# Performance work log

Hardware: AMD Instinct MI355X
Metric: run time of the kernel (lower is better)

## Reference

```python
import jax, jax.numpy as jnp
import numpy as np

N, F_IN, H, OUT, L = 100000, 32, 128, 200, 4
E = 1600000
EPS = 1e-5


def setup_inputs() -> dict:
    key = jax.random.key(0)
    ks = jax.random.split(key, 16)
    glorot = lambda k, shape: jax.random.uniform(k, shape, jnp.float32, -1.0, 1.0) * jnp.sqrt(6.0 / (shape[0] + shape[1]))
    return {
        'x': jax.random.normal(ks[0], (N, F_IN), jnp.float32),
        'edge_index': jax.random.randint(ks[1], (2, E), 0, N, jnp.int32),
        'W_emb': glorot(ks[2], (F_IN, H)), 'b_emb': jnp.zeros((H,), jnp.float32),
        'W_conv': jnp.stack([glorot(jax.random.fold_in(ks[3], i), (H, H)) for i in range(L)]),
        'b_conv': jnp.zeros((L, H), jnp.float32),
        'ln_g': jnp.ones((L, H), jnp.float32), 'ln_b': jnp.zeros((L, H), jnp.float32),
        'W_res': jnp.stack([glorot(jax.random.fold_in(ks[4], i), (H, H)) for i in range(L // 2)]),
        'b_res': jnp.zeros((L // 2, H), jnp.float32),
        'W_fc1': glorot(ks[5], (H, H)), 'b_fc1': jnp.zeros((H,), jnp.float32),
        'fcn_g': jnp.ones((H,), jnp.float32), 'fcn_b': jnp.zeros((H,), jnp.float32),
        'W_fc2': glorot(ks[6], (H, OUT)), 'b_fc2': jnp.zeros((OUT,), jnp.float32),
    }


def _layer_norm(h, g, b):
    mu = jnp.mean(h, axis=-1, keepdims=True)
    var = jnp.mean(jnp.square(h - mu), axis=-1, keepdims=True)
    return (h - mu) * jax.lax.rsqrt(var + EPS) * g + b


def reference(x, edge_index, W_emb, b_emb, W_conv, b_conv, ln_g, ln_b,
              W_res, b_res, W_fc1, b_fc1, fcn_g, fcn_b, W_fc2, b_fc2):
    n = x.shape[0]
    # GCN normalization with self-loops (computed once; same every layer)
    self_idx = jnp.arange(n, dtype=edge_index.dtype)
    src = jnp.concatenate([edge_index[0], self_idx])
    dst = jnp.concatenate([edge_index[1], self_idx])
    deg = jax.ops.segment_sum(jnp.ones_like(src, jnp.float32), dst, num_segments=n)
    dinv = jnp.where(deg > 0, jax.lax.rsqrt(jnp.maximum(deg, 1.0)), 0.0)
    norm = dinv[src] * dinv[dst]  # [E+N]

    h = x @ W_emb + b_emb  # node embedding [N, H]
    for i in range(L):
        residual = (h @ W_res[i // 2 - 1] + b_res[i // 2 - 1]) if (i % 2 == 0 and i > 0) else h
        # GCNConv: transform, gather by src, scale, scatter-add to dst
        ht = h @ W_conv[i]
        msg = norm[:, None] * ht[src]
        h = jax.ops.segment_sum(msg, dst, num_segments=n) + b_conv[i]
        h = jax.nn.relu(_layer_norm(h, ln_g[i], ln_b[i]))
        h = h + residual  # shapes always match ([N, H])
    # no batch vector -> global mean pool over all nodes
    h = jnp.mean(h, axis=0, keepdims=True)  # [1, H]
    h = jax.nn.relu(_layer_norm(h @ W_fc1 + b_fc1, fcn_g, fcn_b))
    return h @ W_fc2 + b_fc2  # [1, OUT]
```

## Files before the change

kernel.cpp:

```cpp
#include <hip/hip_runtime.h>

constexpr int N_NODES = 100000;
constexpr int F_IN    = 32;
constexpr int H       = 128;
constexpr int OUT_F   = 200;
constexpr int NEDGES  = 1600000;
constexpr float EPS   = 1e-5f;

constexpr int TILE_BLKS  = (N_NODES + 63) / 64;
constexpr int MM_BLKS    = TILE_BLKS;
constexpr int MMD_BLKS   = TILE_BLKS * 2;
constexpr int AGG_BLKS   = N_NODES / 32;

constexpr int NB     = (N_NODES + 127) / 128;
constexpr int BCAP   = 2560;
constexpr int P1_EPT = 16, P1_THR = 512;
constexpr int P1_EPB = P1_THR * P1_EPT;
constexpr int P1_BLKS = (NEDGES + P1_EPB - 1) / P1_EPB;
constexpr int WS_BLKS = 40;
constexpr int P2_IT  = BCAP / 256;
constexpr int WQ_BLKS = NEDGES / 4 / 256;

typedef __attribute__((ext_vector_type(8))) short  short8;
typedef __attribute__((ext_vector_type(4))) float  f32x4;
typedef __attribute__((ext_vector_type(2))) float  fv2;

__device__ __forceinline__ void fma4(float4& a, float s, const float4& w) {
  a.x = fmaf(s, w.x, a.x); a.y = fmaf(s, w.y, a.y);
  a.z = fmaf(s, w.z, a.z); a.w = fmaf(s, w.w, a.w);
}

__device__ __forceinline__ unsigned short f2bf(float f) {
  union { float f; unsigned u; } v; v.f = f;
  unsigned r = v.u + 0x7fffu + ((v.u >> 16) & 1u);
  return (unsigned short)(r >> 16);
}
__device__ __forceinline__ float bflo(unsigned u) { return __uint_as_float(u << 16); }
__device__ __forceinline__ float bfhi(unsigned u) { return __uint_as_float(u & 0xffff0000u); }
__device__ __forceinline__ unsigned pack2(float lo, float hi) {
  return (unsigned)f2bf(lo) | ((unsigned)f2bf(hi) << 16);
}
__device__ __forceinline__ void st_bf4(unsigned short* p, float4 v) {
  uint2 o; o.x = pack2(v.x, v.y); o.y = pack2(v.z, v.w);
  *(uint2*)p = o;
}

#if __has_builtin(__builtin_amdgcn_cvt_pk_f32_fp8) && __has_builtin(__builtin_amdgcn_cvt_pk_fp8_f32)
#define HAVE_FP8_CVT 1
#endif

#ifndef HAVE_FP8_CVT
__device__ __forceinline__ float fp8_dec1(unsigned b) {
  unsigned s = (b >> 7) & 1u, E = (b >> 3) & 15u, m = b & 7u;
  float v;
  if (E) {
    union { unsigned u; float f; } t;
    t.u = (s << 31) | ((E + 120u) << 23) | (m << 20);
    v = t.f;
  } else {
    v = (s ? -1.f : 1.f) * (float)m * 0.001953125f;
  }
  return v;
}
#endif

template <bool HI>
__device__ __forceinline__ fv2 fp8x2(unsigned u) {
#ifdef HAVE_FP8_CVT
  return __builtin_amdgcn_cvt_pk_f32_fp8((int)u, HI);
#else
  unsigned p = HI ? (u >> 16) : u;
  fv2 r; r.x = fp8_dec1(p & 0xffu); r.y = fp8_dec1((p >> 8) & 0xffu);
  return r;
#endif
}

__device__ __forceinline__ unsigned char f32_to_fp8(float f) {
#ifdef HAVE_FP8_CVT
  return (unsigned char)(__builtin_amdgcn_cvt_pk_fp8_f32(f, f, 0, false) & 0xff);
#else
  union { float f; unsigned u; } t; t.f = f;
  unsigned s = t.u >> 31;
  float a = fabsf(f);
  if (a > 448.f) a = 448.f;
  t.f = a;
  int e = (int)((t.u >> 23) & 0xff) - 127;
  unsigned char r;
  if (a == 0.f) {
    r = 0;
  } else if (e >= -6) {
    unsigned m = t.u & 0x7fffffu;
    unsigned keep = m >> 20, rest = m & 0xfffffu;
    keep += (rest > 0x80000u) || (rest == 0x80000u && (keep & 1u));
    int E = e + 7;
    if (keep == 8u) { keep = 0u; E += 1; }
    if (E >= 16) { E = 15; keep = 6u; }
    r = (unsigned char)((E << 3) | keep);
  } else {
    int mi = (int)(a * 512.f + 0.5f);
    r = (mi > 7) ? (unsigned char)(1u << 3) : (unsigned char)mi;
  }
  return (unsigned char)(r | (s << 7));
#endif
}

__device__ __forceinline__ void mm_lds_fp8(const unsigned short* sA,
                                           const unsigned short* __restrict__ WT,
                                           int n0, int t,
                                           unsigned char* __restrict__ htOut) {
  int wave = t >> 6, lane = t & 63;
  int wr = wave >> 1, wc = wave & 1;
  int m = lane & 15, quad = (lane >> 4) & 3;
  short8 bh[4][4];
#pragma unroll
  for (int q = 0; q < 4; ++q)
#pragma unroll
    for (int ct = 0; ct < 4; ++ct) {
      int n = wc * 64 + ct * 16 + m;
      bh[q][ct] = *(const short8*)(WT + n * H + q * 32 + quad * 8);
    }
  f32x4 acc[2][4];
#pragma unroll
  for (int i = 0; i < 2; ++i)
#pragma unroll
    for (int j = 0; j < 4; ++j) acc[i][j] = (f32x4){0.f, 0.f, 0.f, 0.f};
#pragma unroll
  for (int q = 0; q < 4; ++q) {
    short8 ah[2];
#pragma unroll
    for (int rt = 0; rt < 2; ++rt)
      ah[rt] = *(const short8*)(sA + (wr * 32 + rt * 16 + m) * 136 + q * 32 + quad * 8);
#pragma unroll
    for (int rt = 0; rt < 2; ++rt)
#pragma unroll
      for (int ct = 0; ct < 4; ++ct)
        acc[rt][ct] = __builtin_amdgcn_mfma_f32_16x16x32_bf16(ah[rt], bh[q][ct], acc[rt][ct], 0, 0, 0);
  }
#pragma unroll
  for (int rt = 0; rt < 2; ++rt)
#pragma unroll
    for (int ct = 0; ct < 4; ++ct) {
      int col = wc * 64 + ct * 16 + m;
#pragma unroll
      for (int rr = 0; rr < 4; ++rr) {
        int gn = n0 + wr * 32 + rt * 16 + quad * 4 + rr;
        if (gn < N_NODES) htOut[(size_t)gn * H + col] = f32_to_fp8(acc[rt][ct][rr]);
      }
    }
}

__global__ __launch_bounds__(256) void k_embed(
    const float* __restrict__ x, const float* __restrict__ W_emb,
    const float* __restrict__ b_emb, unsigned short* __restrict__ h,
    const unsigned short* __restrict__ W0T, unsigned char* __restrict__ ht8) {
  __shared__ __align__(16) char smem[25600];
  int t = threadIdx.x;
  int n0 = blockIdx.x * 64;
  float* sW = (float*)smem;
  float* sX = sW + 4096;
  unsigned short* sH = (unsigned short*)smem;
#pragma unroll
  for (int p = 0; p < 4; ++p)
    ((float4*)sW)[t + p * 256] = ((const float4*)W_emb)[t + p * 256];
#pragma unroll
  for (int p = 0; p < 2; ++p) {
    int fi = t * 2 + p;
    int row = fi >> 3, k4 = (fi & 7) * 4;
    int gn = n0 + row; if (gn >= N_NODES) gn = N_NODES - 1;
    *(float4*)(sX + row * 36 + k4) = *(const float4*)(x + (size_t)gn * F_IN + k4);
  }
  __syncthreads();
  int nr = t >> 2, col0 = (t & 3) * 4;
  float4 acc[8];
#pragma unroll
  for (int i = 0; i < 8; ++i) acc[i] = make_float4(0.f, 0.f, 0.f, 0.f);
#pragma unroll 4
  for (int k = 0; k < F_IN; ++k) {
    float xv = sX[nr * 36 + k];
    const float* wp = sW + k * H + col0;
#pragma unroll
    for (int i = 0; i < 8; ++i) fma4(acc[i], xv, *(const float4*)(wp + i * 16));
  }
#pragma unroll
  for (int i = 0; i < 8; ++i) {
    float4 bv = *(const float4*)(b_emb + col0 + i * 16);
    acc[i].x += bv.x; acc[i].y += bv.y; acc[i].z += bv.z; acc[i].w += bv.w;
  }
  __syncthreads();
  int node = n0 + nr;
  unsigned short* hr = h + (size_t)node * H + col0;
#pragma unroll
  for (int i = 0; i < 8; ++i) {
    st_bf4(sH + nr * 136 + col0 + i * 16, acc[i]);
    if (node < N_NODES) st_bf4(hr + i * 16, acc[i]);
  }
  __syncthreads();
  mm_lds_fp8(sH, W0T, n0, t, ht8);
}

__global__ __launch_bounds__(512) void k_p1(const int* __restrict__ ei,
                                            int* __restrict__ bcnt,
                                            unsigned* __restrict__ bscr,
                                            const float* __restrict__ W_conv,
                                            const float* __restrict__ W_res,
                                            unsigned short* __restrict__ whiT) {
  __shared__ int hist[NB];
  __shared__ int hbase[NB];
  int t = threadIdx.x;
  if (blockIdx.x >= P1_BLKS) {
    int base = (blockIdx.x - P1_BLKS) * 2048;
#pragma unroll
    for (int j = 0; j < 4; ++j) {
      int idx = base + j * 512 + t;
      int m = idx >> 14, rr = idx & 16383;
      int k = rr >> 7, n = rr & 127;
      const float* src = (m < 4) ? (W_conv + m * H * H) : W_res;
      whiT[m * H * H + n * H + k] = f2bf(src[k * H + n]);
    }
    return;
  }
  for (int i = t; i < NB; i += 512) hist[i] = 0;
  __syncthreads();
  int e0 = blockIdx.x * P1_EPB;
  unsigned pk[P1_EPT]; int br[P1_EPT];
#pragma unroll
  for (int k = 0; k < P1_EPT; ++k) {
    int e = e0 + k * 512 + t;
    if (e < NEDGES) {
      int src = ei[e];
      int dst = ei[NEDGES + e];
      int b = dst >> 7;
      pk[k] = ((unsigned)src << 7) | (unsigned)(dst & 127);
      int r = atomicAdd(&hist[b], 1);
      br[k] = (b << 13) | r;
    } else {
      br[k] = -1; pk[k] = 0;
    }
  }
  __syncthreads();
  for (int i = t; i < NB; i += 512) {
    int c = hist[i];
    hbase[i] = c ? atomicAdd(&bcnt[i], c) : 0;
  }
  __syncthreads();
#pragma unroll
  for (int k = 0; k < P1_EPT; ++k) {
    if (br[k] >= 0) {
      int b = br[k] >> 13, r = br[k] & 8191;
      int pos = hbase[b] + r;
      if (pos < BCAP) bscr[(size_t)b * BCAP + pos] = pk[k];
    }
  }
}

__global__ void k_scanbc(const int* __restrict__ bcnt, int* __restrict__ bbase) {
  __shared__ int s[1024];
  int t = threadIdx.x;
  int d = (t < NB) ? bcnt[t] : 0;
  s[t] = d;
  __syncthreads();
#pragma unroll
  for (int off = 1; off < 1024; off <<= 1) {
    int v = (t >= off) ? s[t - off] : 0;
    __syncthreads();
    s[t] += v;
    __syncthreads();
  }
  if (t < NB) bbase[t] = s[t] - d;
}

__global__ __launch_bounds__(256) void k_p2(const unsigned* __restrict__ bscr,
                                            const int* __restrict__ bcnt,
                                            const int* __restrict__ bbase,
                                            int* __restrict__ degT,
                                            int* __restrict__ offs,
                                            float* __restrict__ dinv,
                                            unsigned* __restrict__ csr) {
  __shared__ int dl[128], sc[128];
  int b = blockIdx.x, t = threadIdx.x;
  if (t < 128) dl[t] = 0;
  __syncthreads();
  int n = min(bcnt[b], BCAP);
  int base = bbase[b];
  const unsigned* seg = bscr + (size_t)b * BCAP;
  unsigned pk[P2_IT]; unsigned short rr[P2_IT];
#pragma unroll
  for (int k = 0; k < P2_IT; ++k) {
    int i = k * 256 + t;
    if (i < n) {
      unsigned p = seg[i];
      pk[k] = p;
      rr[k] = (unsigned short)atomicAdd(&dl[p & 127u], 1);
    } else pk[k] = 0xffffffffu;
  }
  __syncthreads();
  if (t < 128) sc[t] = dl[t];
  __syncthreads();
#pragma unroll
  for (int off = 1; off < 128; off <<= 1) {
    int v = (t >= off && t < 128) ? sc[t - off] : 0;
    __syncthreads();
    if (t < 128) sc[t] += v;
    __syncthreads();
  }
  if (t < 128) {
    int node = b * 128 + t;
    if (node < N_NODES) {
      int d = dl[t];
      degT[node] = d;
      dinv[node] = rsqrtf((float)(d + 1));
      offs[node] = base + sc[t] - d;
    }
  }
  __syncthreads();
#pragma unroll
  for (int k = 0; k < P2_IT; ++k) {
    if (pk[k] != 0xffffffffu) {
      unsigned p = pk[k];
      unsigned dlo = p & 127u;
      int pos = base + (sc[dlo] - dl[dlo]) + (int)rr[k];
      csr[pos] = (p >> 7) << 15;
    }
  }
}

__global__ __launch_bounds__(256) void k_wq(unsigned* __restrict__ csr,
                                            const float* __restrict__ dinv) {
  int i = (blockIdx.x * 256 + threadIdx.x) * 4;
  if (i < NEDGES) {
    uint4 e = *(uint4*)(csr + i);
    e.x |= (unsigned)(dinv[e.x >> 15] * 32767.f + 0.5f);
    e.y |= (unsigned)(dinv[e.y >> 15] * 32767.f + 0.5f);
    e.z |= (unsigned)(dinv[e.z >> 15] * 32767.f + 0.5f);
    e.w |= (unsigned)(dinv[e.w >> 15] * 32767.f + 0.5f);
    *(uint4*)(csr + i) = e;
  }
}

__global__ __launch_bounds__(256) void k_mm(const unsigned short* __restrict__ A,
                                            const unsigned short* __restrict__ WhiT,
                                            unsigned char* __restrict__ ht8) {
  __shared__ __align__(16) unsigned short sA[64 * 136];
  int t = threadIdx.x;
  int n0 = blockIdx.x * 64;
#pragma unroll
  for (int p = 0; p < 4; ++p) {
    int fi = t + p * 256;
    int row = fi >> 4, c8 = (fi & 15) * 8;
    int gn = n0 + row; if (gn >= N_NODES) gn = N_NODES - 1;
    *(uint4*)(sA + row * 136 + c8) = *(const uint4*)(A + (size_t)gn * H + c8);
  }
  __syncthreads();
  mm_lds_fp8(sA, WhiT, n0, t, ht8);
}

__global__ __launch_bounds__(256) void k_mmd(const unsigned short* __restrict__ A,
    const unsigned short* __restrict__ WcT, const unsigned short* __restrict__ WrT,
    const float* __restrict__ bias,
    unsigned char* __restrict__ ht8, unsigned short* __restrict__ resb) {
  __shared__ __align__(16) unsigned short sA[64 * 136];
  int t = threadIdx.x;
  int j = blockIdx.x;
  int n0 = (j >> 1) * 64, c0 = (j & 1) * 64;
  int wave = t >> 6, lane = t & 63;
  int wr = wave >> 1, wc = wave & 1;
  int m = lane & 15, quad = (lane >> 4) & 3;
  short8 bhc[4][2], bhr[4][2];
#pragma unroll
  for (int q = 0; q < 4; ++q)
#pragma unroll
    for (int ct = 0; ct < 2; ++ct) {
      int n = c0 + wc * 32 + ct * 16 + m;
      bhc[q][ct] = *(const short8*)(WcT + n * H + q * 32 + quad * 8);
      bhr[q][ct] = *(const short8*)(WrT + n * H + q * 32 + quad * 8);
    }
#pragma unroll
  for (int p = 0; p < 4; ++p) {
    int fi = t + p * 256;
    int row = fi >> 4, c8 = (fi & 15) * 8;
    int gn = n0 + row; if (gn >= N_NODES) gn = N_NODES - 1;
    *(uint4*)(sA + row * 136 + c8) = *(const uint4*)(A + (size_t)gn * H + c8);
  }
  __syncthreads();
  f32x4 accC[2][2], accR[2][2];
#pragma unroll
  for (int i = 0; i < 2; ++i)
#pragma unroll
    for (int jj = 0; jj < 2; ++jj) {
      accC[i][jj] = (f32x4){0.f, 0.f, 0.f, 0.f};
      accR[i][jj] = (f32x4){0.f, 0.f, 0.f, 0.f};
    }
#pragma unroll
  for (int q = 0; q < 4; ++q) {
    short8 ah[2];
#pragma unroll
    for (int rt = 0; rt < 2; ++rt)
      ah[rt] = *(const short8*)(sA + (wr * 32 + rt * 16 + m) * 136 + q * 32 + quad * 8);
#pragma unroll
    for (int rt = 0; rt < 2; ++rt)
#pragma unroll
      for (int ct = 0; ct < 2; ++ct) {
        accC[rt][ct] = __builtin_amdgcn_mfma_f32_16x16x32_bf16(ah[rt], bhc[q][ct], accC[rt][ct], 0, 0, 0);
        accR[rt][ct] = __builtin_amdgcn_mfma_f32_16x16x32_bf16(ah[rt], bhr[q][ct], accR[rt][ct], 0, 0, 0);
      }
  }
#pragma unroll
  for (int rt = 0; rt < 2; ++rt)
#pragma unroll
    for (int ct = 0; ct < 2; ++ct) {
      int col = c0 + wc * 32 + ct * 16 + m;
      float bv = bias[col];
#pragma unroll
      for (int rr = 0; rr < 4; ++rr) {
        int gn = n0 + wr * 32 + rt * 16 + quad * 4 + rr;
        if (gn < N_NODES) {
          ht8[(size_t)gn * H + col]  = f32_to_fp8(accC[rt][ct][rr]);
          resb[(size_t)gn * H + col] = f2bf(accR[rt][ct][rr] + bv);
        }
      }
    }
}

__device__ __forceinline__ void agg_round16(const unsigned char* __restrict__ ht8,
                                            unsigned flo, int gbase,
                                            int s, float w, fv2* acc2) {
  uint2 uu[16]; float ww[16];
#pragma unroll
  for (int jj = 0; jj < 16; ++jj) {
    int ss = __shfl(s, gbase + jj, 64);
    ww[jj] = __shfl(w, gbase + jj, 64);
    uu[jj] = *(const uint2*)(ht8 + (((unsigned)ss << 7) | flo));
  }
#pragma unroll
  for (int jj = 0; jj < 16; ++jj) {
    float we = ww[jj];
    fv2 we2 = {we, we};
    acc2[0] += we2 * fp8x2<false>(uu[jj].x);
    acc2[1] += we2 * fp8x2<true>(uu[jj].x);
    acc2[2] += we2 * fp8x2<false>(uu[jj].y);
    acc2[3] += we2 * fp8x2<true>(uu[jj].y);
  }
}

__global__ __launch_bounds__(512) void k_agg(
    const unsigned char* __restrict__ ht8, const unsigned short* __restrict__ res,
    const float* __restrict__ dinv, const int* __restrict__ offs,
    const int* __restrict__ degT, const unsigned* __restrict__ csr,
    const float* __restrict__ bias, const float* __restrict__ lng,
    const float* __restrict__ lnb, unsigned short* __restrict__ hout) {
  int t = threadIdx.x;
  int fl = t & 15;
  int gbase = t & 48;
  int node = blockIdx.x * 32 + (t >> 4);
  unsigned flo = (unsigned)fl * 8u;
  int start = offs[node], cnt = degT[node];
  float di = dinv[node];
  fv2 acc2[4];
  {
    uint2 u = *(const uint2*)(ht8 + (((unsigned)node << 7) | flo));
    float sw = di * di;
    fv2 sw2 = {sw, sw};
    acc2[0] = sw2 * fp8x2<false>(u.x);
    acc2[1] = sw2 * fp8x2<true>(u.x);
    acc2[2] = sw2 * fp8x2<false>(u.y);
    acc2[3] = sw2 * fp8x2<true>(u.y);
  }
  float ddq = di * (1.f / 32767.f);
  for (int b0 = 0; b0 < cnt; b0 += 16) {
    int s = node; float w = 0.f;
    if (b0 + fl < cnt) {
      unsigned ev = csr[start + b0 + fl];
      s = (int)(ev >> 15);
      w = (float)(ev & 32767u) * ddq;
    }
    agg_round16(ht8, flo, gbase, s, w, acc2);
  }
  float acc[8] = {acc2[0].x, acc2[0].y, acc2[1].x, acc2[1].y,
                  acc2[2].x, acc2[2].y, acc2[3].x, acc2[3].y};
  float4 b0v = *(const float4*)(bias + fl * 8);
  float4 b1v = *(const float4*)(bias + fl * 8 + 4);
  acc[0] += b0v.x; acc[1] += b0v.y; acc[2] += b0v.z; acc[3] += b0v.w;
  acc[4] += b1v.x; acc[5] += b1v.y; acc[6] += b1v.z; acc[7] += b1v.w;
  float sl = ((acc[0] + acc[1]) + (acc[2] + acc[3])) +
             ((acc[4] + acc[5]) + (acc[6] + acc[7]));
#pragma unroll
  for (int mk = 1; mk <= 8; mk <<= 1) sl += __shfl_xor(sl, mk, 16);
  float mu = sl * (1.f / 128.f);
  float d[8];
  float vl = 0.f;
#pragma unroll
  for (int j = 0; j < 8; ++j) { d[j] = acc[j] - mu; vl = fmaf(d[j], d[j], vl); }
#pragma unroll
  for (int mk = 1; mk <= 8; mk <<= 1) vl += __shfl_xor(vl, mk, 16);
  float rs = rsqrtf(vl * (1.f / 128.f) + EPS);
  float4 g0 = *(const float4*)(lng + fl * 8);
  float4 g1 = *(const float4*)(lng + fl * 8 + 4);
  float4 be0 = *(const float4*)(lnb + fl * 8);
  float4 be1 = *(const float4*)(lnb + fl * 8 + 4);
  uint4 rv = *(const uint4*)(res + (size_t)node * 128 + fl * 8);
  float o0 = fmaxf(fmaf(d[0] * rs, g0.x, be0.x), 0.f) + bflo(rv.x);
  float o1 = fmaxf(fmaf(d[1] * rs, g0.y, be0.y), 0.f) + bfhi(rv.x);
  float o2 = fmaxf(fmaf(d[2] * rs, g0.z, be0.z), 0.f) + bflo(rv.y);
  float o3 = fmaxf(fmaf(d[3] * rs, g0.w, be0.w), 0.f) + bfhi(rv.y);
  float o4 = fmaxf(fmaf(d[4] * rs, g1.x, be1.x), 0.f) + bflo(rv.z);
  float o5 = fmaxf(fmaf(d[5] * rs, g1.y, be1.y), 0.f) + bfhi(rv.z);
  float o6 = fmaxf(fmaf(d[6] * rs, g1.z, be1.z), 0.f) + bflo(rv.w);
  float o7 = fmaxf(fmaf(d[7] * rs, g1.w, be1.w), 0.f) + bfhi(rv.w);
  uint4 ov;
  ov.x = pack2(o0, o1); ov.y = pack2(o2, o3);
  ov.z = pack2(o4, o5); ov.w = pack2(o6, o7);
  *(uint4*)(hout + (size_t)node * 128 + fl * 8) = ov;
}

__global__ __launch_bounds__(256) void k_pool(const unsigned short* __restrict__ h,
                                              float* __restrict__ pool) {
  __shared__ float colsum[128];
  int t = threadIdx.x;
  if (t < 128) colsum[t] = 0.f;
  __syncthreads();
  int lr = t >> 4, seg = t & 15;
  float acc[8] = {0.f, 0.f, 0.f, 0.f, 0.f, 0.f, 0.f, 0.f};
  for (int n = blockIdx.x * 16 + lr; n < N_NODES; n += gridDim.x * 16) {
    uint4 u = *(const uint4*)(h + (size_t)n * H + seg * 8);
    acc[0] += bflo(u.x); acc[1] += bfhi(u.x);
    acc[2] += bflo(u.y); acc[3] += bfhi(u.y);
    acc[4] += bflo(u.z); acc[5] += bfhi(u.z);
    acc[6] += bflo(u.w); acc[7] += bfhi(u.w);
  }
#pragma unroll
  for (int j = 0; j < 8; ++j) atomicAdd(&colsum[seg * 8 + j], acc[j]);
  __syncthreads();
  if (t < 128) atomicAdd(&pool[t], colsum[t]);
}

__global__ void k_head(const float* __restrict__ pool, const float* __restrict__ Wfc1,
                       const float* __restrict__ bfc1, const float* __restrict__ g,
                       const float* __restrict__ bb, const float* __restrict__ Wfc2,
                       const float* __restrict__ bfc2, float* __restrict__ out) {
  __shared__ float sm[128], s1[128], stats[2];
  int t = threadIdx.x;
  if (t < 128) sm[t] = pool[t] * (1.f / (float)N_NODES);
  __syncthreads();
  if (t < 128) {
    float a = bfc1[t];
    for (int k = 0; k < 128; ++k) a = fmaf(sm[k], Wfc1[k * 128 + t], a);
    s1[t] = a;
  }
  __syncthreads();
  if (t == 0) {
    float mu = 0.f;
    for (int k = 0; k < 128; ++k) mu += s1[k];
    mu *= (1.f / 128.f);
    float var = 0.f;
    for (int k = 0; k < 128; ++k) { float d = s1[k] - mu; var += d * d; }
    var *= (1.f / 128.f);
    stats[0] = mu; stats[1] = rsqrtf(var + EPS);
  }
  __syncthreads();
  if (t < 128) s1[t] = fmaxf((s1[t] - stats[0]) * stats[1] * g[t] + bb[t], 0.f);
  __syncthreads();
  if (t < OUT_F) {
    float a = bfc2[t];
    for (int k = 0; k < 128; ++k) a = fmaf(s1[k], Wfc2[k * OUT_F + t], a);
    out[t] = a;
  }
}

extern "C" void kernel_launch(void* const* d_in, const int* in_sizes, int n_in,
                              void* d_out, int out_size, void* d_ws, size_t ws_size,
                              hipStream_t stream) {
  const float* x      = (const float*)d_in[0];
  const int*   ei     = (const int*)d_in[1];
  const float* W_emb  = (const float*)d_in[2];
  const float* b_emb  = (const float*)d_in[3];
  const float* W_conv = (const float*)d_in[4];
  const float* b_conv = (const float*)d_in[5];
  const float* ln_g   = (const float*)d_in[6];
  const float* ln_b   = (const float*)d_in[7];
  const float* W_res  = (const float*)d_in[8];
  const float* b_res  = (const float*)d_in[9];
  const float* W_fc1  = (const float*)d_in[10];
  const float* b_fc1  = (const float*)d_in[11];
  const float* fcn_g  = (const float*)d_in[12];
  const float* fcn_b  = (const float*)d_in[13];
  const float* W_fc2  = (const float*)d_in[14];
  const float* b_fc2  = (const float*)d_in[15];
  float* out = (float*)d_out;

  char* p = (char*)d_ws;
  auto take = [&](size_t bytes) {
    char* r = p; p += (bytes + 255) & ~(size_t)255; return r;
  };
  unsigned short* bufA = (unsigned short*)take((size_t)N_NODES * H * 2);
  unsigned short* bufB = (unsigned short*)take((size_t)N_NODES * H * 2);
  unsigned short* bufC = (unsigned short*)take((size_t)N_NODES * H * 2);
  unsigned char*  ht8  = (unsigned char*)take((size_t)N_NODES * H);
  unsigned short* whiT = (unsigned short*)take((size_t)5 * H * H * 2);
  int*   degT = (int*)take(N_NODES * 4);
  int*   offs = (int*)take(N_NODES * 4);
  float* dinv = (float*)take(N_NODES * 4);
  int*   bcnt = (int*)take(NB * 4);
  int*   bbase= (int*)take(NB * 4);
  unsigned* bscr = (unsigned*)take((size_t)NB * BCAP * 4);
  unsigned* csr  = (unsigned*)take((size_t)NEDGES * 4);
  float* pool = (float*)take(128 * 4);

  (void)hipMemsetAsync(bcnt, 0, NB * 4, stream);
  (void)hipMemsetAsync(pool, 0, 128 * 4, stream);

  k_p1<<<P1_BLKS + WS_BLKS, P1_THR, 0, stream>>>(ei, bcnt, bscr,
                                                 W_conv, W_res, whiT);
  k_scanbc<<<1, 1024, 0, stream>>>(bcnt, bbase);
  k_p2<<<NB, 256, 0, stream>>>(bscr, bcnt, bbase, degT, offs, dinv, csr);
  k_wq<<<WQ_BLKS, 256, 0, stream>>>(csr, dinv);
  k_embed<<<TILE_BLKS, 256, 0, stream>>>(x, W_emb, b_emb, bufA,
                                         whiT + 0 * H * H, ht8);

  k_agg<<<AGG_BLKS, 512, 0, stream>>>(ht8, bufA, dinv, offs, degT, csr,
                                      b_conv + 0 * H, ln_g + 0 * H, ln_b + 0 * H, bufC);
  k_mm<<<MM_BLKS, 256, 0, stream>>>(bufC, whiT + 1 * H * H, ht8);
  k_agg<<<AGG_BLKS, 512, 0, stream>>>(ht8, bufC, dinv, offs, degT, csr,
                                      b_conv + 1 * H, ln_g + 1 * H, ln_b + 1 * H, bufA);
  k_mmd<<<MMD_BLKS, 256, 0, stream>>>(bufA, whiT + 2 * H * H, whiT + 4 * H * H,
                                      b_res, ht8, bufB);
  k_agg<<<AGG_BLKS, 512, 0, stream>>>(ht8, bufB, dinv, offs, degT, csr,
                                      b_conv + 2 * H, ln_g + 2 * H, ln_b + 2 * H, bufC);
  k_mm<<<MM_BLKS, 256, 0, stream>>>(bufC, whiT + 3 * H * H, ht8);
  k_agg<<<AGG_BLKS, 512, 0, stream>>>(ht8, bufC, dinv, offs, degT, csr,
                                      b_conv + 3 * H, ln_g + 3 * H, ln_b + 3 * H, bufA);

  k_pool<<<256, 256, 0, stream>>>(bufA, pool);
  k_head<<<1, 256, 0, stream>>>(pool, W_fc1, b_fc1, fcn_g, fcn_b,
                                W_fc2, b_fc2, out);
}
```

Before: 435.5 us.

## Make dense matmul blocks persistent over four tiles with register-prefetched A

k_mm and k_mmd now process four 64-row tiles per block instead of one. Each block loads the weight B-fragments into registers once and reuses them across the tiles, and it prefetches the next tile's A rows into registers while the current tile's MFMAs run. This reduces redundant weight loads and exposes load/compute overlap. The cost is a quarter as many blocks, so occupancy and parallelism across CUs drop, and k_mm now holds 16 short8 B fragments in registers.

```diff
diff --git a/kernel.cpp b/kernel.cpp
--- a/kernel.cpp
+++ b/kernel.cpp
@@ -8,8 +8,9 @@
 constexpr float EPS   = 1e-5f;
 
 constexpr int TILE_BLKS  = (N_NODES + 63) / 64;
-constexpr int MM_BLKS    = TILE_BLKS;
-constexpr int MMD_BLKS   = TILE_BLKS * 2;
+constexpr int MMT        = 4;
+constexpr int MM_BLKS    = (TILE_BLKS + MMT - 1) / MMT;
+constexpr int MMD_BLKS   = MM_BLKS * 2;
 constexpr int AGG_BLKS   = N_NODES / 32;
 
 constexpr int NB     = (N_NODES + 127) / 128;
@@ -342,16 +343,64 @@
                                             unsigned char* __restrict__ ht8) {
   __shared__ __align__(16) unsigned short sA[64 * 136];
   int t = threadIdx.x;
-  int n0 = blockIdx.x * 64;
-#pragma unroll
-  for (int p = 0; p < 4; ++p) {
-    int fi = t + p * 256;
-    int row = fi >> 4, c8 = (fi & 15) * 8;
-    int gn = n0 + row; if (gn >= N_NODES) gn = N_NODES - 1;
-    *(uint4*)(sA + row * 136 + c8) = *(const uint4*)(A + (size_t)gn * H + c8);
-  }
-  __syncthreads();
-  mm_lds_fp8(sA, WhiT, n0, t, ht8);
+  int wave = t >> 6, lane = t & 63;
+  int wr = wave >> 1, wc = wave & 1;
+  int m = lane & 15, quad = (lane >> 4) & 3;
+  short8 bh[4][4];
+#pragma unroll
+  for (int q = 0; q < 4; ++q)
+#pragma unroll
+    for (int ct = 0; ct < 4; ++ct)
+      bh[q][ct] = *(const short8*)(WhiT + (wc * 64 + ct * 16 + m) * H + q * 32 + quad * 8);
+  int srow = t >> 4, sc8 = (t & 15) * 8;
+  int tbase = blockIdx.x * MMT;
+  int nt = min(MMT, TILE_BLKS - tbase);
+  uint4 rg[4];
+  auto ldA = [&](int n0) {
+#pragma unroll
+    for (int p = 0; p < 4; ++p) {
+      int gn = n0 + srow + 16 * p; if (gn >= N_NODES) gn = N_NODES - 1;
+      rg[p] = *(const uint4*)(A + (size_t)gn * H + sc8);
+    }
+  };
+  ldA(tbase * 64);
+  for (int tt = 0; tt < nt; ++tt) {
+    int n0 = (tbase + tt) * 64;
+#pragma unroll
+    for (int p = 0; p < 4; ++p)
+      *(uint4*)(sA + (srow + 16 * p) * 136 + sc8) = rg[p];
+    __syncthreads();
+    if (tt + 1 < nt) ldA(n0 + 64);
+    f32x4 acc[2][4];
+#pragma unroll
+    for (int i = 0; i < 2; ++i)
+#pragma unroll
+      for (int j = 0; j < 4; ++j) acc[i][j] = (f32x4){0.f, 0.f, 0.f, 0.f};
+#pragma unroll
+    for (int q = 0; q < 4; ++q) {
+      short8 ah[2];
+#pragma unroll
+      for (int rt = 0; rt < 2; ++rt)
+        ah[rt] = *(const short8*)(sA + (wr * 32 + rt * 16 + m) * 136 + q * 32 + quad * 8);
+#pragma unroll
+      for (int rt = 0; rt < 2; ++rt)
+#pragma unroll
+        for (int ct = 0; ct < 4; ++ct)
+          acc[rt][ct] = __builtin_amdgcn_mfma_f32_16x16x32_bf16(ah[rt], bh[q][ct], acc[rt][ct], 0, 0, 0);
+    }
+#pragma unroll
+    for (int rt = 0; rt < 2; ++rt)
+#pragma unroll
+      for (int ct = 0; ct < 4; ++ct) {
+        int col = wc * 64 + ct * 16 + m;
+#pragma unroll
+        for (int rr = 0; rr < 4; ++rr) {
+          int gn = n0 + wr * 32 + rt * 16 + quad * 4 + rr;
+          if (gn < N_NODES) ht8[(size_t)gn * H + col] = f32_to_fp8(acc[rt][ct][rr]);
+        }
+      }
+    __syncthreads();
+  }
 }
 
 __global__ __launch_bounds__(256) void k_mmd(const unsigned short* __restrict__ A,
@@ -360,8 +409,9 @@
     unsigned char* __restrict__ ht8, unsigned short* __restrict__ resb) {
   __shared__ __align__(16) unsigned short sA[64 * 136];
   int t = threadIdx.x;
-  int j = blockIdx.x;
-  int n0 = (j >> 1) * 64, c0 = (j & 1) * 64;
+  int c0 = (blockIdx.x & 1) * 64;
+  int tbase = (blockIdx.x >> 1) * MMT;
+  int nt = min(MMT, TILE_BLKS - tbase);
   int wave = t >> 6, lane = t & 63;
   int wr = wave >> 1, wc = wave & 1;
   int m = lane & 15, quad = (lane >> 4) & 3;
@@ -374,51 +424,62 @@
       bhc[q][ct] = *(const short8*)(WcT + n * H + q * 32 + quad * 8);
       bhr[q][ct] = *(const short8*)(WrT + n * H + q * 32 + quad * 8);
     }
-#pragma unroll
-  for (int p = 0; p < 4; ++p) {
-    int fi = t + p * 256;
-    int row = fi >> 4, c8 = (fi & 15) * 8;
-    int gn = n0 + row; if (gn >= N_NODES) gn = N_NODES - 1;
-    *(uint4*)(sA + row * 136 + c8) = *(const uint4*)(A + (size_t)gn * H + c8);
-  }
-  __syncthreads();
-  f32x4 accC[2][2], accR[2][2];
-#pragma unroll
-  for (int i = 0; i < 2; ++i)
-#pragma unroll
-    for (int jj = 0; jj < 2; ++jj) {
-      accC[i][jj] = (f32x4){0.f, 0.f, 0.f, 0.f};
-      accR[i][jj] = (f32x4){0.f, 0.f, 0.f, 0.f};
-    }
-#pragma unroll
-  for (int q = 0; q < 4; ++q) {
-    short8 ah[2];
+  int srow = t >> 4, sc8 = (t & 15) * 8;
+  uint4 rg[4];
+  auto ldA = [&](int n0) {
+#pragma unroll
+    for (int p = 0; p < 4; ++p) {
+      int gn = n0 + srow + 16 * p; if (gn >= N_NODES) gn = N_NODES - 1;
+      rg[p] = *(const uint4*)(A + (size_t)gn * H + sc8);
+    }
+  };
+  ldA(tbase * 64);
+  for (int tt = 0; tt < nt; ++tt) {
+    int n0 = (tbase + tt) * 64;
+#pragma unroll
+    for (int p = 0; p < 4; ++p)
+      *(uint4*)(sA + (srow + 16 * p) * 136 + sc8) = rg[p];
+    __syncthreads();
+    if (tt + 1 < nt) ldA(n0 + 64);
+    f32x4 accC[2][2], accR[2][2];
+#pragma unroll
+    for (int i = 0; i < 2; ++i)
+#pragma unroll
+      for (int jj = 0; jj < 2; ++jj) {
+        accC[i][jj] = (f32x4){0.f, 0.f, 0.f, 0.f};
+        accR[i][jj] = (f32x4){0.f, 0.f, 0.f, 0.f};
+      }
+#pragma unroll
+    for (int q = 0; q < 4; ++q) {
+      short8 ah[2];
+#pragma unroll
+      for (int rt = 0; rt < 2; ++rt)
+        ah[rt] = *(const short8*)(sA + (wr * 32 + rt * 16 + m) * 136 + q * 32 + quad * 8);
+#pragma unroll
+      for (int rt = 0; rt < 2; ++rt)
+#pragma unroll
+        for (int ct = 0; ct < 2; ++ct) {
+          accC[rt][ct] = __builtin_amdgcn_mfma_f32_16x16x32_bf16(ah[rt], bhc[q][ct], accC[rt][ct], 0, 0, 0);
+          accR[rt][ct] = __builtin_amdgcn_mfma_f32_16x16x32_bf16(ah[rt], bhr[q][ct], accR[rt][ct], 0, 0, 0);
+        }
+    }
 #pragma unroll
     for (int rt = 0; rt < 2; ++rt)
-      ah[rt] = *(const short8*)(sA + (wr * 32 + rt * 16 + m) * 136 + q * 32 + quad * 8);
-#pragma unroll
-    for (int rt = 0; rt < 2; ++rt)
 #pragma unroll
       for (int ct = 0; ct < 2; ++ct) {
-        accC[rt][ct] = __builtin_amdgcn_mfma_f32_16x16x32_bf16(ah[rt], bhc[q][ct], accC[rt][ct], 0, 0, 0);
-        accR[rt][ct] = __builtin_amdgcn_mfma_f32_16x16x32_bf16(ah[rt], bhr[q][ct], accR[rt][ct], 0, 0, 0);
-      }
-  }
-#pragma unroll
-  for (int rt = 0; rt < 2; ++rt)
-#pragma unroll
-    for (int ct = 0; ct < 2; ++ct) {
-      int col = c0 + wc * 32 + ct * 16 + m;
-      float bv = bias[col];
-#pragma unroll
-      for (int rr = 0; rr < 4; ++rr) {
-        int gn = n0 + wr * 32 + rt * 16 + quad * 4 + rr;
-        if (gn < N_NODES) {
-          ht8[(size_t)gn * H + col]  = f32_to_fp8(accC[rt][ct][rr]);
-          resb[(size_t)gn * H + col] = f2bf(accR[rt][ct][rr] + bv);
+        int col = c0 + wc * 32 + ct * 16 + m;
+        float bv = bias[col];
+#pragma unroll
+        for (int rr = 0; rr < 4; ++rr) {
+          int gn = n0 + wr * 32 + rt * 16 + quad * 4 + rr;
+          if (gn < N_NODES) {
+            ht8[(size_t)gn * H + col]  = f32_to_fp8(accC[rt][ct][rr]);
+            resb[(size_t)gn * H + col] = f2bf(accR[rt][ct][rr] + bv);
+          }
         }
       }
-    }
+    __syncthreads();
+  }
 }
 
 __device__ __forceinline__ void agg_round16(const unsigned char* __restrict__ ht8,
```

Result: no change. 436.1 us (+0.1%).

## Fuse next-layer GEMM into aggregation epilogue and loop tiles in k_mmd

Applied to the files above, without the earlier changes.

The aggregation kernel gains a templated epilogue. After the layer-norm output is written, it stages the 32-row tile in LDS and runs the next layer's 128x128 MFMA transform, writing fp8 features into a second ping-pong buffer. This removes the standalone k_mm launches and the reread of the bf16 activations. Separately, k_mmd now processes four 64-row tiles per block, prefetching the next tile into registers while computing, so the weight fragments are loaded once per block. The fused path adds LDS use, a block barrier and register pressure to the latency-bound gather kernel, which could reduce its occupancy.

```diff
diff --git a/kernel.cpp b/kernel.cpp
--- a/kernel.cpp
+++ b/kernel.cpp
@@ -8,8 +8,8 @@
 constexpr float EPS   = 1e-5f;
 
 constexpr int TILE_BLKS  = (N_NODES + 63) / 64;
-constexpr int MM_BLKS    = TILE_BLKS;
-constexpr int MMD_BLKS   = TILE_BLKS * 2;
+constexpr int MMT        = 4;
+constexpr int MMD_BLKS   = ((TILE_BLKS + MMT - 1) / MMT) * 2;
 constexpr int AGG_BLKS   = N_NODES / 32;
 
 constexpr int NB     = (N_NODES + 127) / 128;
@@ -337,31 +337,15 @@
   }
 }
 
-__global__ __launch_bounds__(256) void k_mm(const unsigned short* __restrict__ A,
-                                            const unsigned short* __restrict__ WhiT,
-                                            unsigned char* __restrict__ ht8) {
-  __shared__ __align__(16) unsigned short sA[64 * 136];
-  int t = threadIdx.x;
-  int n0 = blockIdx.x * 64;
-#pragma unroll
-  for (int p = 0; p < 4; ++p) {
-    int fi = t + p * 256;
-    int row = fi >> 4, c8 = (fi & 15) * 8;
-    int gn = n0 + row; if (gn >= N_NODES) gn = N_NODES - 1;
-    *(uint4*)(sA + row * 136 + c8) = *(const uint4*)(A + (size_t)gn * H + c8);
-  }
-  __syncthreads();
-  mm_lds_fp8(sA, WhiT, n0, t, ht8);
-}
-
 __global__ __launch_bounds__(256) void k_mmd(const unsigned short* __restrict__ A,
     const unsigned short* __restrict__ WcT, const unsigned short* __restrict__ WrT,
     const float* __restrict__ bias,
     unsigned char* __restrict__ ht8, unsigned short* __restrict__ resb) {
   __shared__ __align__(16) unsigned short sA[64 * 136];
   int t = threadIdx.x;
-  int j = blockIdx.x;
-  int n0 = (j >> 1) * 64, c0 = (j & 1) * 64;
+  int c0 = (blockIdx.x & 1) * 64;
+  int tbase = (blockIdx.x >> 1) * MMT;
+  int nt = min(MMT, TILE_BLKS - tbase);
   int wave = t >> 6, lane = t & 63;
   int wr = wave >> 1, wc = wave & 1;
   int m = lane & 15, quad = (lane >> 4) & 3;
@@ -374,51 +358,62 @@
       bhc[q][ct] = *(const short8*)(WcT + n * H + q * 32 + quad * 8);
       bhr[q][ct] = *(const short8*)(WrT + n * H + q * 32 + quad * 8);
     }
-#pragma unroll
-  for (int p = 0; p < 4; ++p) {
-    int fi = t + p * 256;
-    int row = fi >> 4, c8 = (fi & 15) * 8;
-    int gn = n0 + row; if (gn >= N_NODES) gn = N_NODES - 1;
-    *(uint4*)(sA + row * 136 + c8) = *(const uint4*)(A + (size_t)gn * H + c8);
-  }
-  __syncthreads();
-  f32x4 accC[2][2], accR[2][2];
-#pragma unroll
-  for (int i = 0; i < 2; ++i)
-#pragma unroll
-    for (int jj = 0; jj < 2; ++jj) {
-      accC[i][jj] = (f32x4){0.f, 0.f, 0.f, 0.f};
-      accR[i][jj] = (f32x4){0.f, 0.f, 0.f, 0.f};
-    }
-#pragma unroll
-  for (int q = 0; q < 4; ++q) {
-    short8 ah[2];
+  int srow = t >> 4, sc8 = (t & 15) * 8;
+  uint4 rg[4];
+  auto ldA = [&](int n0) {
+#pragma unroll
+    for (int p = 0; p < 4; ++p) {
+      int gn = n0 + srow + 16 * p; if (gn >= N_NODES) gn = N_NODES - 1;
+      rg[p] = *(const uint4*)(A + (size_t)gn * H + sc8);
+    }
+  };
+  ldA(tbase * 64);
+  for (int tt = 0; tt < nt; ++tt) {
+    int n0 = (tbase + tt) * 64;
+#pragma unroll
+    for (int p = 0; p < 4; ++p)
+      *(uint4*)(sA + (srow + 16 * p) * 136 + sc8) = rg[p];
+    __syncthreads();
+    if (tt + 1 < nt) ldA(n0 + 64);
+    f32x4 accC[2][2], accR[2][2];
+#pragma unroll
+    for (int i = 0; i < 2; ++i)
+#pragma unroll
+      for (int jj = 0; jj < 2; ++jj) {
+        accC[i][jj] = (f32x4){0.f, 0.f, 0.f, 0.f};
+        accR[i][jj] = (f32x4){0.f, 0.f, 0.f, 0.f};
+      }
+#pragma unroll
+    for (int q = 0; q < 4; ++q) {
+      short8 ah[2];
+#pragma unroll
+      for (int rt = 0; rt < 2; ++rt)
+        ah[rt] = *(const short8*)(sA + (wr * 32 + rt * 16 + m) * 136 + q * 32 + quad * 8);
+#pragma unroll
+      for (int rt = 0; rt < 2; ++rt)
+#pragma unroll
+        for (int ct = 0; ct < 2; ++ct) {
+          accC[rt][ct] = __builtin_amdgcn_mfma_f32_16x16x32_bf16(ah[rt], bhc[q][ct], accC[rt][ct], 0, 0, 0);
+          accR[rt][ct] = __builtin_amdgcn_mfma_f32_16x16x32_bf16(ah[rt], bhr[q][ct], accR[rt][ct], 0, 0, 0);
+        }
+    }
 #pragma unroll
     for (int rt = 0; rt < 2; ++rt)
-      ah[rt] = *(const short8*)(sA + (wr * 32 + rt * 16 + m) * 136 + q * 32 + quad * 8);
-#pragma unroll
-    for (int rt = 0; rt < 2; ++rt)
 #pragma unroll
       for (int ct = 0; ct < 2; ++ct) {
-        accC[rt][ct] = __builtin_amdgcn_mfma_f32_16x16x32_bf16(ah[rt], bhc[q][ct], accC[rt][ct], 0, 0, 0);
-        accR[rt][ct] = __builtin_amdgcn_mfma_f32_16x16x32_bf16(ah[rt], bhr[q][ct], accR[rt][ct], 0, 0, 0);
-      }
-  }
-#pragma unroll
-  for (int rt = 0; rt < 2; ++rt)
-#pragma unroll
-    for (int ct = 0; ct < 2; ++ct) {
-      int col = c0 + wc * 32 + ct * 16 + m;
-      float bv = bias[col];
-#pragma unroll
-      for (int rr = 0; rr < 4; ++rr) {
-        int gn = n0 + wr * 32 + rt * 16 + quad * 4 + rr;
-        if (gn < N_NODES) {
-          ht8[(size_t)gn * H + col]  = f32_to_fp8(accC[rt][ct][rr]);
-          resb[(size_t)gn * H + col] = f2bf(accR[rt][ct][rr] + bv);
+        int col = c0 + wc * 32 + ct * 16 + m;
+        float bv = bias[col];
+#pragma unroll
+        for (int rr = 0; rr < 4; ++rr) {
+          int gn = n0 + wr * 32 + rt * 16 + quad * 4 + rr;
+          if (gn < N_NODES) {
+            ht8[(size_t)gn * H + col]  = f32_to_fp8(accC[rt][ct][rr]);
+            resb[(size_t)gn * H + col] = f2bf(accR[rt][ct][rr] + bv);
+          }
         }
       }
-    }
+    __syncthreads();
+  }
 }
 
 __device__ __forceinline__ void agg_round16(const unsigned char* __restrict__ ht8,
@@ -442,22 +437,26 @@
   }
 }
 
-__global__ __launch_bounds__(512) void k_agg(
-    const unsigned char* __restrict__ ht8, const unsigned short* __restrict__ res,
+template <bool FUSE>
+__global__ __launch_bounds__(512) void k_aggT(
+    const unsigned char* __restrict__ ht8_in, const unsigned short* __restrict__ res,
     const float* __restrict__ dinv, const int* __restrict__ offs,
     const int* __restrict__ degT, const unsigned* __restrict__ csr,
     const float* __restrict__ bias, const float* __restrict__ lng,
-    const float* __restrict__ lnb, unsigned short* __restrict__ hout) {
+    const float* __restrict__ lnb, unsigned short* __restrict__ hout,
+    const unsigned short* __restrict__ WT, unsigned char* __restrict__ ht8_out) {
+  __shared__ __align__(16) unsigned short sH[FUSE ? 32 * 136 : 16];
   int t = threadIdx.x;
   int fl = t & 15;
   int gbase = t & 48;
-  int node = blockIdx.x * 32 + (t >> 4);
+  int lr = t >> 4;
+  int node = blockIdx.x * 32 + lr;
   unsigned flo = (unsigned)fl * 8u;
   int start = offs[node], cnt = degT[node];
   float di = dinv[node];
   fv2 acc2[4];
   {
-    uint2 u = *(const uint2*)(ht8 + (((unsigned)node << 7) | flo));
+    uint2 u = *(const uint2*)(ht8_in + (((unsigned)node << 7) | flo));
     float sw = di * di;
     fv2 sw2 = {sw, sw};
     acc2[0] = sw2 * fp8x2<false>(u.x);
@@ -473,7 +472,7 @@
       s = (int)(ev >> 15);
       w = (float)(ev & 32767u) * ddq;
     }
-    agg_round16(ht8, flo, gbase, s, w, acc2);
+    agg_round16(ht8_in, flo, gbase, s, w, acc2);
   }
   float acc[8] = {acc2[0].x, acc2[0].y, acc2[1].x, acc2[1].y,
                   acc2[2].x, acc2[2].y, acc2[3].x, acc2[3].y};
@@ -510,6 +509,38 @@
   ov.x = pack2(o0, o1); ov.y = pack2(o2, o3);
   ov.z = pack2(o4, o5); ov.w = pack2(o6, o7);
   *(uint4*)(hout + (size_t)node * 128 + fl * 8) = ov;
+  if constexpr (FUSE) {
+    *(uint4*)(sH + lr * 136 + fl * 8) = ov;
+    int wave = t >> 6, lane = t & 63;
+    int m = lane & 15, quad = (lane >> 4) & 3;
+    int r0 = (wave >> 2) * 16;
+    int c0 = (wave & 3) * 32;
+    short8 bh[2][4];
+#pragma unroll
+    for (int ct = 0; ct < 2; ++ct)
+#pragma unroll
+      for (int q = 0; q < 4; ++q)
+        bh[ct][q] = *(const short8*)(WT + (c0 + ct * 16 + m) * H + q * 32 + quad * 8);
+    __syncthreads();
+    f32x4 macc[2];
+#pragma unroll
+    for (int ct = 0; ct < 2; ++ct) macc[ct] = (f32x4){0.f, 0.f, 0.f, 0.f};
+#pragma unroll
+    for (int q = 0; q < 4; ++q) {
+      short8 ah = *(const short8*)(sH + (r0 + m) * 136 + q * 32 + quad * 8);
+#pragma unroll
+      for (int ct = 0; ct < 2; ++ct)
+        macc[ct] = __builtin_amdgcn_mfma_f32_16x16x32_bf16(ah, bh[ct][q], macc[ct], 0, 0, 0);
+    }
+    int gr = blockIdx.x * 32 + r0 + quad * 4;
+#pragma unroll
+    for (int ct = 0; ct < 2; ++ct) {
+      int col = c0 + ct * 16 + m;
+#pragma unroll
+      for (int rr = 0; rr < 4; ++rr)
+        ht8_out[(size_t)(gr + rr) * H + col] = f32_to_fp8(macc[ct][rr]);
+    }
+  }
 }
 
 __global__ __launch_bounds__(256) void k_pool(const unsigned short* __restrict__ h,
@@ -591,10 +622,10 @@
   auto take = [&](size_t bytes) {
     char* r = p; p += (bytes + 255) & ~(size_t)255; return r;
   };
-  unsigned short* bufA = (unsigned short*)take((size_t)N_NODES * H * 2);
-  unsigned short* bufB = (unsigned short*)take((size_t)N_NODES * H * 2);
-  unsigned short* bufC = (unsigned short*)take((size_t)N_NODES * H * 2);
-  unsigned char*  ht8  = (unsigned char*)take((size_t)N_NODES * H);
+  unsigned short* bufX = (unsigned short*)take((size_t)N_NODES * H * 2);
+  unsigned short* bufY = (unsigned short*)take((size_t)N_NODES * H * 2);
+  unsigned char*  ht8A = (unsigned char*)take((size_t)N_NODES * H);
+  unsigned char*  ht8B = (unsigned char*)take((size_t)N_NODES * H);
   unsigned short* whiT = (unsigned short*)take((size_t)5 * H * H * 2);
   int*   degT = (int*)take(N_NODES * 4);
   int*   offs = (int*)take(N_NODES * 4);
@@ -613,23 +644,25 @@
   k_scanbc<<<1, 1024, 0, stream>>>(bcnt, bbase);
   k_p2<<<NB, 256, 0, stream>>>(bscr, bcnt, bbase, degT, offs, dinv, csr);
   k_wq<<<WQ_BLKS, 256, 0, stream>>>(csr, dinv);
-  k_embed<<<TILE_BLKS, 256, 0, stream>>>(x, W_emb, b_emb, bufA,
-                                         whiT + 0 * H * H, ht8);
-
-  k_agg<<<AGG_BLKS, 512, 0, stream>>>(ht8, bufA, dinv, offs, degT, csr,
-                                      b_conv + 0 * H, ln_g + 0 * H, ln_b + 0 * H, bufC);
-  k_mm<<<MM_BLKS, 256, 0, stream>>>(bufC, whiT + 1 * H * H, ht8);
-  k_agg<<<AGG_BLKS, 512, 0, stream>>>(ht8, bufC, dinv, offs, degT, csr,
-                                      b_conv + 1 * H, ln_g + 1 * H, ln_b + 1 * H, bufA);
-  k_mmd<<<MMD_BLKS, 256, 0, stream>>>(bufA, whiT + 2 * H * H, whiT + 4 * H * H,
-                                      b_res, ht8, bufB);
-  k_agg<<<AGG_BLKS, 512, 0, stream>>>(ht8, bufB, dinv, offs, degT, csr,
-                                      b_conv + 2 * H, ln_g + 2 * H, ln_b + 2 * H, bufC);
-  k_mm<<<MM_BLKS, 256, 0, stream>>>(bufC, whiT + 3 * H * H, ht8);
-  k_agg<<<AGG_BLKS, 512, 0, stream>>>(ht8, bufC, dinv, offs, degT, csr,
-                                      b_conv + 3 * H, ln_g + 3 * H, ln_b + 3 * H, bufA);
-
-  k_pool<<<256, 256, 0, stream>>>(bufA, pool);
+  k_embed<<<TILE_BLKS, 256, 0, stream>>>(x, W_emb, b_emb, bufX,
+                                         whiT + 0 * H * H, ht8A);
+
+  k_aggT<true><<<AGG_BLKS, 512, 0, stream>>>(ht8A, bufX, dinv, offs, degT, csr,
+                                             b_conv + 0 * H, ln_g + 0 * H, ln_b + 0 * H,
+                                             bufY, whiT + 1 * H * H, ht8B);
+  k_aggT<false><<<AGG_BLKS, 512, 0, stream>>>(ht8B, bufY, dinv, offs, degT, csr,
+                                              b_conv + 1 * H, ln_g + 1 * H, ln_b + 1 * H,
+                                              bufX, nullptr, nullptr);
+  k_mmd<<<MMD_BLKS, 256, 0, stream>>>(bufX, whiT + 2 * H * H, whiT + 4 * H * H,
+                                      b_res, ht8A, bufY);
+  k_aggT<true><<<AGG_BLKS, 512, 0, stream>>>(ht8A, bufY, dinv, offs, degT, csr,
+                                             b_conv + 2 * H, ln_g + 2 * H, ln_b + 2 * H,
+                                             bufX, whiT + 3 * H * H, ht8B);
+  k_aggT<false><<<AGG_BLKS, 512, 0, stream>>>(ht8B, bufX, dinv, offs, degT, csr,
+                                              b_conv + 3 * H, ln_g + 3 * H, ln_b + 3 * H,
+                                              bufY, nullptr, nullptr);
+
+  k_pool<<<256, 256, 0, stream>>>(bufY, pool);
   k_head<<<1, 256, 0, stream>>>(pool, W_fc1, b_fc1, fcn_g, fcn_b,
                                 W_fc2, b_fc2, out);
 }
```

After: 440.2 us. About the same (+1.1%).
